# Kernel tuning notes

Measured on AMD Instinct MI355X. Metric: run time of the kernel, lower is better.

## Reference

```python
import jax, jax.numpy as jnp
import numpy as np

# config constants (match init_kwargs)
K_MAX = 32
T = 0.1
EPS = 1e-08


def setup_inputs() -> dict:
    key = jax.random.key(0)
    k1, k2, k3 = jax.random.split(key, 3)
    S, d_k, d_A = 8, 128, 1024
    B, N = 256, 100000
    scale = d_A ** (-0.5)
    return {
        "z": jax.random.normal(k1, (B, d_A), dtype=jnp.float32),
        "pool_keys": jax.random.normal(k2, (S, N, d_k), dtype=jnp.float32),
        "W_Q": jax.random.normal(k3, (S, d_k, d_A), dtype=jnp.float32) * scale,
        "aspect_weights": jnp.zeros((S,), dtype=jnp.float32),
        "tau": jnp.asarray(0.0, dtype=jnp.float32),
        "lambda_val": jnp.asarray(10.0, dtype=jnp.float32),
        "is_warmup": jnp.asarray(False),
    }


def reference(z, pool_keys, W_Q, aspect_weights, tau, lambda_val, is_warmup):
    # queries: [B, S, d_k]
    queries = jnp.einsum('ska,ba->bsk', W_Q, z)
    qn = queries / (jnp.linalg.norm(queries, axis=-1, keepdims=True) + EPS)
    kn = pool_keys / (jnp.linalg.norm(pool_keys, axis=-1, keepdims=True) + EPS)
    # per-aspect cosine similarity: [B, S, N]
    sim = jnp.einsum('bsk,snk->bsn', qn, kn)
    w = jax.nn.softmax(aspect_weights, axis=0)  # [S]
    s_i = jnp.einsum('s,bsn->bn', w, sim)       # [B, N]

    def warmup_select(_):
        scores, idx = jax.lax.top_k(s_i, K_MAX)
        alpha = jax.nn.softmax(scores / T, axis=-1)
        return (alpha, idx)

    def gate_select(_):
        g = jax.nn.sigmoid(lambda_val * (s_i - tau))
        raw = g * jnp.exp(s_i / T)
        raw = raw / (raw.sum(axis=-1, keepdims=True) + EPS)
        top_raw, idx = jax.lax.top_k(raw, K_MAX)
        alpha = top_raw / (top_raw.sum(axis=-1, keepdims=True) + EPS)
        return (alpha, idx)

    alphas, indices = jax.lax.cond(is_warmup, warmup_select, gate_select, None)
    return (alphas, indices)
```

## Files before the change

### kernel.cpp

```cpp
#include <hip/hip_runtime.h>
#include <hip/hip_bf16.h>
#include <hip/hip_fp8.h>
#include <math.h>

#define B_      256
#define DA      1024
#define S_      8
#define DK      128
#define NKEYS   100000
#define KMAX    32
#define KTOT    1024
#define BN      128
#define BK      64
#define NBLK    ((NKEYS + BN - 1) / BN)
#define GB      8
#define ZCH     256
#define NA_BLK  (B_ / GB * S_)
#define NK_BLK  ((S_ * NKEYS) / 16)
#define BLK_PER_ASPECT (NKEYS / 16)
#define KSCALE  16.0f
#define QSCALE  4.0f

typedef __attribute__((ext_vector_type(8))) short short8;
typedef __attribute__((ext_vector_type(4))) float f32x4;

typedef const __attribute__((address_space(1))) unsigned gu32;
typedef __attribute__((address_space(3))) unsigned lu32;
#define GLOAD_LDS16(g, s) __builtin_amdgcn_global_load_lds((gu32*)(g), (lu32*)(s), 16, 0, 0)

__device__ __forceinline__ float bf16_up(short h) {
    union { unsigned u; float f; } cv;
    cv.u = ((unsigned)(unsigned short)h) << 16;
    return cv.f;
}
__device__ __forceinline__ unsigned char f32_to_e4m3(float x) {
    __hip_fp8_e4m3 h(x);
    return (unsigned char)h.__x;
}

__global__ void pass_w_kernel(const float* __restrict__ aw, float* __restrict__ W8)
{
    if (threadIdx.x == 0 && blockIdx.x == 0) {
        float mx = aw[0];
        #pragma unroll
        for (int i = 1; i < S_; ++i) mx = fmaxf(mx, aw[i]);
        float e[S_]; float se = 0.f;
        #pragma unroll
        for (int i = 0; i < S_; ++i) { e[i] = expf(aw[i] - mx); se += e[i]; }
        #pragma unroll
        for (int i = 0; i < S_; ++i) W8[i] = e[i] / se;
    }
}

__global__ __launch_bounds__(256) void pass_ak_kernel(
    const float* __restrict__ z, const float* __restrict__ wq,
    const float* __restrict__ keys, const float* __restrict__ W8,
    float* __restrict__ QT, unsigned char* __restrict__ Q8,
    float* __restrict__ F, unsigned char* __restrict__ K8)
{
    __shared__ float zsh[GB][ZCH];
    __shared__ double part[2];

    if (blockIdx.x < NA_BLK) {
        const int ab = blockIdx.x;
        const int b0 = (ab & (B_ / GB - 1)) * GB;
        const int s  = ab >> 5;
        const int tid = threadIdx.x;
        const int k = tid & 127;
        const bool act = tid < 128;
        const float* wrow = wq + (size_t)(s * DK + k) * DA;
        double acc[GB] = {};

        for (int ch = 0; ch < DA; ch += ZCH) {
            __syncthreads();
            for (int i = tid; i < GB * ZCH; i += 256)
                zsh[i >> 8][i & (ZCH - 1)] =
                    z[(size_t)(b0 + (i >> 8)) * DA + ch + (i & (ZCH - 1))];
            __syncthreads();
            if (act) {
                for (int a = 0; a < ZCH; a += 32) {
                    float4 w[8];
                    #pragma unroll
                    for (int j = 0; j < 8; ++j)
                        w[j] = *reinterpret_cast<const float4*>(wrow + ch + a + 4 * j);
                    #pragma unroll
                    for (int j = 0; j < 8; ++j) {
                        const int aa = a + 4 * j;
                        #pragma unroll
                        for (int g = 0; g < GB; ++g) {
                            acc[g] += (double)w[j].x * (double)zsh[g][aa + 0];
                            acc[g] += (double)w[j].y * (double)zsh[g][aa + 1];
                            acc[g] += (double)w[j].z * (double)zsh[g][aa + 2];
                            acc[g] += (double)w[j].w * (double)zsh[g][aa + 3];
                        }
                    }
                }
            }
        }
        #pragma unroll
        for (int g = 0; g < GB; ++g) {
            double sq = acc[g] * acc[g];
            #pragma unroll
            for (int off = 32; off > 0; off >>= 1) sq += __shfl_down(sq, off);
            if (act && (tid & 63) == 0) part[tid >> 6] = sq;
            __syncthreads();
            const double ss  = part[0] + part[1];
            const double inv = 1.0 / (sqrt(ss) + 1e-8);
            if (act) {
                const float qv = (float)(acc[g] * inv);
                QT[(size_t)(s * DK + k) * B_ + b0 + g] = qv;
                Q8[(size_t)(b0 + g) * KTOT + s * DK + k] = f32_to_e4m3(qv * QSCALE);
            }
            __syncthreads();
        }
    } else {
        const int brel = blockIdx.x - NA_BLK;
        const int g = threadIdx.x >> 4, l = threadIdx.x & 15;
        const int s = brel / BLK_PER_ASPECT;
        const long long sn = (long long)brel * 16 + g;
        const float* row = keys + (size_t)sn * DK + l * 8;
        const float4 r0 = *reinterpret_cast<const float4*>(row + 0);
        const float4 r1 = *reinterpret_cast<const float4*>(row + 4);
        double sq = (double)r0.x * r0.x + (double)r0.y * r0.y +
                    (double)r0.z * r0.z + (double)r0.w * r0.w +
                    (double)r1.x * r1.x + (double)r1.y * r1.y +
                    (double)r1.z * r1.z + (double)r1.w * r1.w;
        #pragma unroll
        for (int off = 1; off < 16; off <<= 1) sq += __shfl_xor(sq, off);
        const float w = W8[s];
        const float f = (float)((double)w / (sqrt(sq) + 1e-8));
        if (l == 0) F[sn] = f;

        const float fs = f * KSCALE;
        int lo = 0, hi = 0;
        lo = __builtin_amdgcn_cvt_pk_fp8_f32(r0.x * fs, r0.y * fs, lo, false);
        lo = __builtin_amdgcn_cvt_pk_fp8_f32(r0.z * fs, r0.w * fs, lo, true);
        hi = __builtin_amdgcn_cvt_pk_fp8_f32(r1.x * fs, r1.y * fs, hi, false);
        hi = __builtin_amdgcn_cvt_pk_fp8_f32(r1.z * fs, r1.w * fs, hi, true);
        const unsigned long long pk =
            ((unsigned long long)(unsigned)hi << 32) | (unsigned)lo;
        *reinterpret_cast<unsigned long long*>(K8 + (size_t)sn * DK + l * 8) = pk;
    }
}

__global__ __launch_bounds__(512) void pass_b_kernel(
    const unsigned char* __restrict__ K8, const unsigned char* __restrict__ Q8,
    __hip_bfloat16* __restrict__ C)
{
    __shared__ __align__(16) char smem[32768];
    const int n0 = blockIdx.x * BN;
    const int tid = threadIdx.x;
    const int w = tid >> 6, l = tid & 63;
    const int ln = l & 15, lk = l >> 4;
    const int wm = w >> 1, wn = w & 1;
    const int lr = l >> 2;
    const int gg = (l & 3) * 2;

    f32x4 acc[4][4];
    #pragma unroll
    for (int i = 0; i < 4; ++i)
        #pragma unroll
        for (int j = 0; j < 4; ++j) acc[i][j] = (f32x4){0.f, 0.f, 0.f, 0.f};

    const char* q8 = (const char*)Q8;
    const char* k8 = (const char*)K8;

    auto stage_b = [&](int t) {
        const int kc   = t * BK;
        const int sidx = kc >> 7;
        const int kl   = kc & (DK - 1);
        const int nr   = w * 16 + lr;
        const size_t gn = (size_t)sidx * NKEYS + (n0 + nr);
        const char* g = k8 + gn * DK + kl + ((gg ^ (nr & 6)) << 3);
        GLOAD_LDS16(g, smem + 16384 + (t & 1) * 8192 + w * 1024);
    };

    stage_b(0);

    for (int t = 0; t < 16; ++t) {
        const int kc = t * BK;
        #pragma unroll
        for (int i = 0; i < 2; ++i) {
            const int j  = w + 8 * i;
            const int bq = j * 16 + lr;
            const char* g = q8 + (size_t)bq * KTOT + kc + ((gg ^ (bq & 6)) << 3);
            GLOAD_LDS16(g, smem + j * 1024);
        }
        stage_b(t + 1);
        asm volatile("s_waitcnt vmcnt(1)" ::: "memory");
        __builtin_amdgcn_sched_barrier(0);
        __builtin_amdgcn_s_barrier();
        __builtin_amdgcn_sched_barrier(0);
        const char* bbase = smem + 16384 + (t & 1) * 8192;
        #pragma unroll
        for (int kw = 0; kw < 2; ++kw) {
            const int slot = kw * 4 + lk;
            long af[4], bf[4];
            #pragma unroll
            for (int mi = 0; mi < 4; ++mi) {
                const int r = wm * 64 + mi * 16 + ln;
                af[mi] = *reinterpret_cast<const long*>(smem + r * 64 + ((slot ^ (r & 6)) << 3));
            }
            #pragma unroll
            for (int nf = 0; nf < 4; ++nf) {
                const int nr = wn * 64 + nf * 16 + ln;
                bf[nf] = *reinterpret_cast<const long*>(bbase + nr * 64 + ((slot ^ (nr & 6)) << 3));
            }
            #pragma unroll
            for (int mi = 0; mi < 4; ++mi)
                #pragma unroll
                for (int nf = 0; nf < 4; ++nf)
                    acc[mi][nf] = __builtin_amdgcn_mfma_f32_16x16x32_fp8_fp8(
                        af[mi], bf[nf], acc[mi][nf], 0, 0, 0);
        }
        __builtin_amdgcn_s_barrier();
    }
    asm volatile("s_waitcnt vmcnt(0)" ::: "memory");

    #pragma unroll
    for (int mi = 0; mi < 4; ++mi) {
        #pragma unroll
        for (int nf = 0; nf < 4; ++nf) {
            const int n = n0 + wn * 64 + nf * 16 + ln;
            if (n < NKEYS) {
                #pragma unroll
                for (int r = 0; r < 4; ++r) {
                    const int bq = wm * 64 + mi * 16 + lk * 4 + r;
                    C[(size_t)bq * NKEYS + n] = __float2bfloat16(acc[mi][nf][r]);
                }
            }
        }
    }
}

#define MAXC 2048
#define NV8 12500
#define NSS (NV8 / 8)
#define CTH 512

__global__ __launch_bounds__(512) void pass_c_kernel(
    const __hip_bfloat16* __restrict__ C, const float* __restrict__ keys,
    const float* __restrict__ QT, const float* __restrict__ F,
    const float* __restrict__ tau_p, const float* __restrict__ lam_p,
    const unsigned char* __restrict__ warm_p, float* __restrict__ out)
{
    const int b = blockIdx.x, tid = threadIdx.x;
    __shared__ float redA[8], redB[8];
    __shared__ double cval[MAXC];
    __shared__ int cidx[MAXC];
    __shared__ int cnt;
    __shared__ float sh_stat[2];
    __shared__ double topv[KMAX];
    __shared__ int topi[KMAX];

    const __hip_bfloat16* crow = C + (size_t)b * NKEYS;

    float sm = 0.f, sq = 0.f;
    for (int ii = tid; ii < NSS; ii += 2 * CTH) {
        const short8 v0 = *reinterpret_cast<const short8*>(crow + (size_t)ii * 64);
        const bool ok1 = (ii + CTH) < NSS;
        short8 v1 = v0;
        if (ok1) v1 = *reinterpret_cast<const short8*>(crow + (size_t)(ii + CTH) * 64);
        #pragma unroll
        for (int e = 0; e < 8; ++e) {
            const float v = bf16_up(v0[e]);
            sm += v; sq += v * v;
        }
        if (ok1) {
            #pragma unroll
            for (int e = 0; e < 8; ++e) {
                const float v = bf16_up(v1[e]);
                sm += v; sq += v * v;
            }
        }
    }
    #pragma unroll
    for (int off = 32; off > 0; off >>= 1) {
        sm += __shfl_down(sm, off);
        sq += __shfl_down(sq, off);
    }
    if ((tid & 63) == 0) { redA[tid >> 6] = sm; redB[tid >> 6] = sq; }
    __syncthreads();
    if (tid == 0) {
        float S1 = 0.f, S2 = 0.f;
        #pragma unroll
        for (int i = 0; i < 8; ++i) { S1 += redA[i]; S2 += redB[i]; }
        const float nsv = (float)(NSS * 8);
        const float mu = S1 / nsv;
        sh_stat[0] = mu;
        sh_stat[1] = sqrtf(fmaxf(S2 / nsv - mu * mu, 1e-12f));
    }
    __syncthreads();
    const float mu = sh_stat[0], sg = sh_stat[1];

    int m = 0;
    #pragma unroll 1
    for (int attempt = 0; attempt < 4; ++attempt) {
        const float ct = (attempt == 0) ? (mu + 3.0f * sg)
                       : (attempt == 1) ? (mu + 2.5f * sg)
                       : (attempt == 2) ? mu : -1e9f;
        __syncthreads();
        if (tid == 0) cnt = 0;
        __syncthreads();
        int i = tid;
        for (; i + 3 * CTH < NV8; i += 4 * CTH) {
            const short8 v0 = *reinterpret_cast<const short8*>(crow + (size_t)(i          ) * 8);
            const short8 v1 = *reinterpret_cast<const short8*>(crow + (size_t)(i +     CTH) * 8);
            const short8 v2 = *reinterpret_cast<const short8*>(crow + (size_t)(i + 2 * CTH) * 8);
            const short8 v3 = *reinterpret_cast<const short8*>(crow + (size_t)(i + 3 * CTH) * 8);
            #pragma unroll
            for (int e = 0; e < 8; ++e)
                if (bf16_up(v0[e]) >= ct) {
                    const int p = atomicAdd(&cnt, 1);
                    if (p < MAXC) cidx[p] = i * 8 + e;
                }
            #pragma unroll
            for (int e = 0; e < 8; ++e)
                if (bf16_up(v1[e]) >= ct) {
                    const int p = atomicAdd(&cnt, 1);
                    if (p < MAXC) cidx[p] = (i + CTH) * 8 + e;
                }
            #pragma unroll
            for (int e = 0; e < 8; ++e)
                if (bf16_up(v2[e]) >= ct) {
                    const int p = atomicAdd(&cnt, 1);
                    if (p < MAXC) cidx[p] = (i + 2 * CTH) * 8 + e;
                }
            #pragma unroll
            for (int e = 0; e < 8; ++e)
                if (bf16_up(v3[e]) >= ct) {
                    const int p = atomicAdd(&cnt, 1);
                    if (p < MAXC) cidx[p] = (i + 3 * CTH) * 8 + e;
                }
        }
        for (; i < NV8; i += CTH) {
            const short8 v8 = *reinterpret_cast<const short8*>(crow + (size_t)i * 8);
            #pragma unroll
            for (int e = 0; e < 8; ++e)
                if (bf16_up(v8[e]) >= ct) {
                    const int p = atomicAdd(&cnt, 1);
                    if (p < MAXC) cidx[p] = i * 8 + e;
                }
        }
        __syncthreads();
        m = min(cnt, MAXC);
        if (m >= KMAX) break;
    }

    const int wave = tid >> 6, lane = tid & 63;
    const int si = lane >> 3, kg = lane & 7;
    for (int c = wave; c < m; c += 8) {
        const int n = cidx[c];
        const float f = F[(size_t)si * NKEYS + n];
        const float* krow = keys + ((size_t)si * NKEYS + n) * DK + kg * 16;
        const float* qb = QT + (size_t)(si * DK + kg * 16) * B_ + b;
        double acc = 0.0;
        #pragma unroll
        for (int jj = 0; jj < 4; ++jj) {
            const float4 kv = *reinterpret_cast<const float4*>(krow + jj * 4);
            acc += (double)qb[(size_t)(jj * 4 + 0) * B_] * ((double)kv.x * (double)f);
            acc += (double)qb[(size_t)(jj * 4 + 1) * B_] * ((double)kv.y * (double)f);
            acc += (double)qb[(size_t)(jj * 4 + 2) * B_] * ((double)kv.z * (double)f);
            acc += (double)qb[(size_t)(jj * 4 + 3) * B_] * ((double)kv.w * (double)f);
        }
        #pragma unroll
        for (int off = 1; off < 64; off <<= 1) acc += __shfl_xor(acc, off);
        if (lane == 0) cval[c] = acc;
    }
    __syncthreads();

    if (tid < 64) {
        for (int r = 0; r < KMAX; ++r) {
            double bv = -1e300; int bi = 0x7fffffff; int bp = -1;
            for (int c = tid; c < m; c += 64) {
                const double v = cval[c]; const int ix = cidx[c];
                if (v > bv || (v == bv && ix < bi)) { bv = v; bi = ix; bp = c; }
            }
            #pragma unroll
            for (int off = 32; off > 0; off >>= 1) {
                const double ov = __shfl_xor(bv, off);
                const int oi = __shfl_xor(bi, off);
                const int op = __shfl_xor(bp, off);
                if (ov > bv || (ov == bv && oi < bi)) { bv = ov; bi = oi; bp = op; }
            }
            if (tid == 0) { topv[r] = bv; topi[r] = bi; if (bp >= 0) cval[bp] = -1e301; }
        }
        if (tid == 0) {
            const float lamv = lam_p[0];
            const float tauv = tau_p[0];
            const bool warm = warm_p[0] != 0;
            float al[KMAX];
            float ssum = 0.f;
            if (warm) {
                const float x0 = (float)topv[0] / 0.1f;
                for (int i = 0; i < KMAX; ++i) {
                    const float e = expf((float)topv[i] / 0.1f - x0);
                    al[i] = e; ssum += e;
                }
            } else {
                for (int i = 0; i < KMAX; ++i) {
                    const float v = (float)topv[i];
                    const float g = 1.0f / (1.0f + expf(-(lamv * (v - tauv))));
                    const float rr = g * expf(v / 0.1f);
                    al[i] = rr; ssum += rr;
                }
            }
            for (int i = 0; i < KMAX; ++i) {
                out[b * KMAX + i] = al[i] / ssum;
                out[B_ * KMAX + b * KMAX + i] = (float)topi[i];
            }
        }
    }
}

extern "C" void kernel_launch(void* const* d_in, const int* in_sizes, int n_in,
                              void* d_out, int out_size, void* d_ws, size_t ws_size,
                              hipStream_t stream) {
    const float* z    = (const float*)d_in[0];
    const float* keys = (const float*)d_in[1];
    const float* wq   = (const float*)d_in[2];
    const float* aw   = (const float*)d_in[3];
    const float* tau  = (const float*)d_in[4];
    const float* lam  = (const float*)d_in[5];
    const unsigned char* warm = (const unsigned char*)d_in[6];
    float* out = (float*)d_out;

    char* ws = (char*)d_ws;
    float* QT           = (float*)ws;
    float* F            = (float*)(ws + (1 << 20));
    float* W8           = (float*)(ws + (5 << 20));
    unsigned char* Q8   = (unsigned char*)(ws + (8 << 20));
    unsigned char* K8   = (unsigned char*)(ws + (16 << 20));
    __hip_bfloat16* C   = (__hip_bfloat16*)(ws + ((size_t)232 << 20));

    pass_w_kernel<<<dim3(1), 64, 0, stream>>>(aw, W8);
    pass_ak_kernel<<<dim3(NA_BLK + NK_BLK), 256, 0, stream>>>(z, wq, keys, W8, QT, Q8, F, K8);
    pass_b_kernel<<<dim3(NBLK), 512, 0, stream>>>(K8, Q8, C);
    pass_c_kernel<<<dim3(B_), 512, 0, stream>>>(C, keys, QT, F, tau, lam, warm, out);
}
```

Before: 279.3 us.

## Split candidate scan into a 4-way parallel kernel ahead of refinement pass

The per-row threshold scan over the bf16 similarity row is moved into a separate kernel launched with four blocks per row, each scanning a quarter of the row. Candidates are appended to a global list through global atomics. The refinement kernel then reuses that list and only rescans with lower thresholds when too few candidates were found. This raises parallelism beyond 256 blocks for the memory-bound scan. In exchange it adds a memset, an extra launch, recomputes the row statistics in every quarter-block, and uses global atomics.

```diff
diff --git a/kernel.cpp b/kernel.cpp
--- a/kernel.cpp
+++ b/kernel.cpp
@@ -238,9 +238,102 @@
 #define NSS (NV8 / 8)
 #define CTH 512
 
-__global__ __launch_bounds__(512) void pass_c_kernel(
+__global__ __launch_bounds__(512) void pass_cs_kernel(
+    const __hip_bfloat16* __restrict__ C,
+    int* __restrict__ CNT, int* __restrict__ CIDX)
+{
+    const int b = blockIdx.x, q = blockIdx.y, tid = threadIdx.x;
+    __shared__ float redA[8], redB[8];
+    __shared__ float sh_stat[2];
+
+    const __hip_bfloat16* crow = C + (size_t)b * NKEYS;
+
+    float sm = 0.f, sq = 0.f;
+    for (int ii = tid; ii < NSS; ii += 2 * CTH) {
+        const short8 v0 = *reinterpret_cast<const short8*>(crow + (size_t)ii * 64);
+        const bool ok1 = (ii + CTH) < NSS;
+        short8 v1 = v0;
+        if (ok1) v1 = *reinterpret_cast<const short8*>(crow + (size_t)(ii + CTH) * 64);
+        #pragma unroll
+        for (int e = 0; e < 8; ++e) {
+            const float v = bf16_up(v0[e]);
+            sm += v; sq += v * v;
+        }
+        if (ok1) {
+            #pragma unroll
+            for (int e = 0; e < 8; ++e) {
+                const float v = bf16_up(v1[e]);
+                sm += v; sq += v * v;
+            }
+        }
+    }
+    #pragma unroll
+    for (int off = 32; off > 0; off >>= 1) {
+        sm += __shfl_down(sm, off);
+        sq += __shfl_down(sq, off);
+    }
+    if ((tid & 63) == 0) { redA[tid >> 6] = sm; redB[tid >> 6] = sq; }
+    __syncthreads();
+    if (tid == 0) {
+        float S1 = 0.f, S2 = 0.f;
+        #pragma unroll
+        for (int i = 0; i < 8; ++i) { S1 += redA[i]; S2 += redB[i]; }
+        const float nsv = (float)(NSS * 8);
+        const float mu = S1 / nsv;
+        sh_stat[0] = mu;
+        sh_stat[1] = sqrtf(fmaxf(S2 / nsv - mu * mu, 1e-12f));
+    }
+    __syncthreads();
+    const float ct = sh_stat[0] + 3.0f * sh_stat[1];
+
+    const int lo = q * (NV8 / 4), hi = (q + 1) * (NV8 / 4);
+    int* cil = CIDX + (size_t)b * MAXC;
+    int i = lo + tid;
+    for (; i + 3 * CTH < hi; i += 4 * CTH) {
+        const short8 v0 = *reinterpret_cast<const short8*>(crow + (size_t)(i          ) * 8);
+        const short8 v1 = *reinterpret_cast<const short8*>(crow + (size_t)(i +     CTH) * 8);
+        const short8 v2 = *reinterpret_cast<const short8*>(crow + (size_t)(i + 2 * CTH) * 8);
+        const short8 v3 = *reinterpret_cast<const short8*>(crow + (size_t)(i + 3 * CTH) * 8);
+        #pragma unroll
+        for (int e = 0; e < 8; ++e)
+            if (bf16_up(v0[e]) >= ct) {
+                const int p = atomicAdd(&CNT[b], 1);
+                if (p < MAXC) cil[p] = i * 8 + e;
+            }
+        #pragma unroll
+        for (int e = 0; e < 8; ++e)
+            if (bf16_up(v1[e]) >= ct) {
+                const int p = atomicAdd(&CNT[b], 1);
+                if (p < MAXC) cil[p] = (i + CTH) * 8 + e;
+            }
+        #pragma unroll
+        for (int e = 0; e < 8; ++e)
+            if (bf16_up(v2[e]) >= ct) {
+                const int p = atomicAdd(&CNT[b], 1);
+                if (p < MAXC) cil[p] = (i + 2 * CTH) * 8 + e;
+            }
+        #pragma unroll
+        for (int e = 0; e < 8; ++e)
+            if (bf16_up(v3[e]) >= ct) {
+                const int p = atomicAdd(&CNT[b], 1);
+                if (p < MAXC) cil[p] = (i + 3 * CTH) * 8 + e;
+            }
+    }
+    for (; i < hi; i += CTH) {
+        const short8 v8 = *reinterpret_cast<const short8*>(crow + (size_t)i * 8);
+        #pragma unroll
+        for (int e = 0; e < 8; ++e)
+            if (bf16_up(v8[e]) >= ct) {
+                const int p = atomicAdd(&CNT[b], 1);
+                if (p < MAXC) cil[p] = i * 8 + e;
+            }
+    }
+}
+
+__global__ __launch_bounds__(512) void pass_r_kernel(
     const __hip_bfloat16* __restrict__ C, const float* __restrict__ keys,
     const float* __restrict__ QT, const float* __restrict__ F,
+    const int* __restrict__ CNT, const int* __restrict__ CIDX,
     const float* __restrict__ tau_p, const float* __restrict__ lam_p,
     const unsigned char* __restrict__ warm_p, float* __restrict__ out)
 {
@@ -255,96 +348,62 @@
 
     const __hip_bfloat16* crow = C + (size_t)b * NKEYS;
 
-    float sm = 0.f, sq = 0.f;
-    for (int ii = tid; ii < NSS; ii += 2 * CTH) {
-        const short8 v0 = *reinterpret_cast<const short8*>(crow + (size_t)ii * 64);
-        const bool ok1 = (ii + CTH) < NSS;
-        short8 v1 = v0;
-        if (ok1) v1 = *reinterpret_cast<const short8*>(crow + (size_t)(ii + CTH) * 64);
-        #pragma unroll
-        for (int e = 0; e < 8; ++e) {
-            const float v = bf16_up(v0[e]);
-            sm += v; sq += v * v;
-        }
-        if (ok1) {
-            #pragma unroll
-            for (int e = 0; e < 8; ++e) {
-                const float v = bf16_up(v1[e]);
-                sm += v; sq += v * v;
-            }
-        }
-    }
-    #pragma unroll
-    for (int off = 32; off > 0; off >>= 1) {
-        sm += __shfl_down(sm, off);
-        sq += __shfl_down(sq, off);
-    }
-    if ((tid & 63) == 0) { redA[tid >> 6] = sm; redB[tid >> 6] = sq; }
-    __syncthreads();
-    if (tid == 0) {
-        float S1 = 0.f, S2 = 0.f;
-        #pragma unroll
-        for (int i = 0; i < 8; ++i) { S1 += redA[i]; S2 += redB[i]; }
-        const float nsv = (float)(NSS * 8);
-        const float mu = S1 / nsv;
-        sh_stat[0] = mu;
-        sh_stat[1] = sqrtf(fmaxf(S2 / nsv - mu * mu, 1e-12f));
-    }
-    __syncthreads();
-    const float mu = sh_stat[0], sg = sh_stat[1];
-
-    int m = 0;
-    #pragma unroll 1
-    for (int attempt = 0; attempt < 4; ++attempt) {
-        const float ct = (attempt == 0) ? (mu + 3.0f * sg)
-                       : (attempt == 1) ? (mu + 2.5f * sg)
-                       : (attempt == 2) ? mu : -1e9f;
+    int m = min(CNT[b], MAXC);
+    if (m >= KMAX) {
+        for (int c = tid; c < m; c += CTH) cidx[c] = CIDX[(size_t)b * MAXC + c];
         __syncthreads();
-        if (tid == 0) cnt = 0;
+    } else {
+        float sm = 0.f, sq = 0.f;
+        for (int ii = tid; ii < NSS; ii += 2 * CTH) {
+            const short8 v0 = *reinterpret_cast<const short8*>(crow + (size_t)ii * 64);
+            const bool ok1 = (ii + CTH) < NSS;
+            short8 v1 = v0;
+            if (ok1) v1 = *reinterpret_cast<const short8*>(crow + (size_t)(ii + CTH) * 64);
+            #pragma unroll
+            for (int e = 0; e < 8; ++e) { const float v = bf16_up(v0[e]); sm += v; sq += v * v; }
+            if (ok1) {
+                #pragma unroll
+                for (int e = 0; e < 8; ++e) { const float v = bf16_up(v1[e]); sm += v; sq += v * v; }
+            }
+        }
+        #pragma unroll
+        for (int off = 32; off > 0; off >>= 1) {
+            sm += __shfl_down(sm, off);
+            sq += __shfl_down(sq, off);
+        }
+        if ((tid & 63) == 0) { redA[tid >> 6] = sm; redB[tid >> 6] = sq; }
         __syncthreads();
-        int i = tid;
-        for (; i + 3 * CTH < NV8; i += 4 * CTH) {
-            const short8 v0 = *reinterpret_cast<const short8*>(crow + (size_t)(i          ) * 8);
-            const short8 v1 = *reinterpret_cast<const short8*>(crow + (size_t)(i +     CTH) * 8);
-            const short8 v2 = *reinterpret_cast<const short8*>(crow + (size_t)(i + 2 * CTH) * 8);
-            const short8 v3 = *reinterpret_cast<const short8*>(crow + (size_t)(i + 3 * CTH) * 8);
-            #pragma unroll
-            for (int e = 0; e < 8; ++e)
-                if (bf16_up(v0[e]) >= ct) {
-                    const int p = atomicAdd(&cnt, 1);
-                    if (p < MAXC) cidx[p] = i * 8 + e;
-                }
-            #pragma unroll
-            for (int e = 0; e < 8; ++e)
-                if (bf16_up(v1[e]) >= ct) {
-                    const int p = atomicAdd(&cnt, 1);
-                    if (p < MAXC) cidx[p] = (i + CTH) * 8 + e;
-                }
-            #pragma unroll
-            for (int e = 0; e < 8; ++e)
-                if (bf16_up(v2[e]) >= ct) {
-                    const int p = atomicAdd(&cnt, 1);
-                    if (p < MAXC) cidx[p] = (i + 2 * CTH) * 8 + e;
-                }
-            #pragma unroll
-            for (int e = 0; e < 8; ++e)
-                if (bf16_up(v3[e]) >= ct) {
-                    const int p = atomicAdd(&cnt, 1);
-                    if (p < MAXC) cidx[p] = (i + 3 * CTH) * 8 + e;
-                }
-        }
-        for (; i < NV8; i += CTH) {
-            const short8 v8 = *reinterpret_cast<const short8*>(crow + (size_t)i * 8);
-            #pragma unroll
-            for (int e = 0; e < 8; ++e)
-                if (bf16_up(v8[e]) >= ct) {
-                    const int p = atomicAdd(&cnt, 1);
-                    if (p < MAXC) cidx[p] = i * 8 + e;
-                }
+        if (tid == 0) {
+            float S1 = 0.f, S2 = 0.f;
+            #pragma unroll
+            for (int i = 0; i < 8; ++i) { S1 += redA[i]; S2 += redB[i]; }
+            const float nsv = (float)(NSS * 8);
+            const float mu = S1 / nsv;
+            sh_stat[0] = mu;
+            sh_stat[1] = sqrtf(fmaxf(S2 / nsv - mu * mu, 1e-12f));
         }
         __syncthreads();
-        m = min(cnt, MAXC);
-        if (m >= KMAX) break;
+        const float mu = sh_stat[0], sg = sh_stat[1];
+        #pragma unroll 1
+        for (int attempt = 0; attempt < 3; ++attempt) {
+            const float ct = (attempt == 0) ? (mu + 2.5f * sg)
+                           : (attempt == 1) ? mu : -1e9f;
+            __syncthreads();
+            if (tid == 0) cnt = 0;
+            __syncthreads();
+            for (int i = tid; i < NV8; i += CTH) {
+                const short8 v8 = *reinterpret_cast<const short8*>(crow + (size_t)i * 8);
+                #pragma unroll
+                for (int e = 0; e < 8; ++e)
+                    if (bf16_up(v8[e]) >= ct) {
+                        const int p = atomicAdd(&cnt, 1);
+                        if (p < MAXC) cidx[p] = i * 8 + e;
+                    }
+            }
+            __syncthreads();
+            m = min(cnt, MAXC);
+            if (m >= KMAX) break;
+        }
     }
 
     const int wave = tid >> 6, lane = tid & 63;
@@ -428,13 +487,17 @@
     char* ws = (char*)d_ws;
     float* QT           = (float*)ws;
     float* F            = (float*)(ws + (1 << 20));
-    float* W8           = (float*)(ws + (5 << 20));
-    unsigned char* Q8   = (unsigned char*)(ws + (8 << 20));
+    int* CNT            = (int*)(ws + (5 << 20));
+    float* W8           = (float*)(ws + (5 << 20) + 4096);
+    int* CIDX           = (int*)(ws + (6 << 20));
+    unsigned char* Q8   = (unsigned char*)(ws + (9 << 20));
     unsigned char* K8   = (unsigned char*)(ws + (16 << 20));
     __hip_bfloat16* C   = (__hip_bfloat16*)(ws + ((size_t)232 << 20));
 
+    hipMemsetAsync(CNT, 0, B_ * sizeof(int), stream);
     pass_w_kernel<<<dim3(1), 64, 0, stream>>>(aw, W8);
     pass_ak_kernel<<<dim3(NA_BLK + NK_BLK), 256, 0, stream>>>(z, wq, keys, W8, QT, Q8, F, K8);
     pass_b_kernel<<<dim3(NBLK), 512, 0, stream>>>(K8, Q8, C);
-    pass_c_kernel<<<dim3(B_), 512, 0, stream>>>(C, keys, QT, F, tau, lam, warm, out);
-}
+    pass_cs_kernel<<<dim3(B_, 4), 512, 0, stream>>>(C, CNT, CIDX);
+    pass_r_kernel<<<dim3(B_), 512, 0, stream>>>(C, keys, QT, F, CNT, CIDX, tau, lam, warm, out);
+}
```

Result: slower. 322.7 us (+15.5%).
